# Kernel optimization log

Measured on AMD Instinct MI355X. Metric: run time of the kernel, lower is better.

The kernel has to match this reference:

```python
import jax, jax.numpy as jnp
import numpy as np
from functools import partial

DT = 1e-3
TAU_SYN_INV = 200.0  # norse default 1/5e-3
TAU_MEM_INV = 100.0  # norse default 1/1e-2

@partial(jax.custom_vjp, nondiff_argnums=(1,))
def superspike(x, alpha):
    return (x > 0).astype(x.dtype)

def _ss_fwd(x, alpha):
    return (x > 0).astype(x.dtype), x

def _ss_bwd(alpha, x, g):
    return (g / (alpha * jnp.abs(x) + 1.0) ** 2,)

superspike.defvjp(_ss_fwd, _ss_bwd)

def conv2d(x, w, b):
    y = jax.lax.conv_general_dilated(x, w, (1, 1), 'VALID',
                                     dimension_numbers=('NCHW', 'OIHW', 'NCHW'))
    return y + b[None, :, None, None]

def maxpool3(x):
    return jax.lax.reduce_window(x, -jnp.inf, jax.lax.max,
                                 (1, 1, 3, 3), (1, 1, 3, 3), 'VALID')

def lif_ff(inp, state, v_th, alpha):
    # norse feed-forward LIF: decay v and i, spike, reset, inject input current
    v, i = state
    v_dec = v + DT * TAU_MEM_INV * (-v + i)   # v_leak = 0
    i_dec = i - DT * TAU_SYN_INV * i
    z = superspike(v_dec - v_th, alpha)
    v_new = (1.0 - z) * v_dec                  # v_reset = 0
    return z, (v_new, i_dec + inp)

def lif_rec(inp, state, w_in, w_rec, v_th, alpha):
    # norse recurrent LIF: recurrent current uses PREVIOUS step's spikes
    z, v, i = state
    v_dec = v + DT * TAU_MEM_INV * (-v + i)
    i_dec = i - DT * TAU_SYN_INV * i
    z_new = superspike(v_dec - v_th, alpha)
    v_new = (1.0 - z_new) * v_dec
    i_new = i_dec + inp @ w_in.T + z @ w_rec.T
    return z_new, (z_new, v_new, i_new)

def li(inp, state):
    # leaky integrator readout (no spiking)
    v, i = state
    v_new = v + DT * TAU_MEM_INV * (-v + i)
    i_new = i - DT * TAU_SYN_INV * i + inp
    return v_new, (v_new, i_new)

def setup_inputs() -> dict:
    key = jax.random.key(0)
    ks = jax.random.split(key, 9)
    B, T, C, H, W = 32, 150, 2, 34, 34
    HID = 512
    x = jax.random.uniform(ks[0], (B, T, C, H, W), dtype=jnp.float32)
    def w(k, shape, fan_in):
        return jax.random.normal(k, shape, dtype=jnp.float32) / np.float32(np.sqrt(fan_in))
    return {
        'x': x,
        'conv1_w': w(ks[1], (30, 2, 7, 7), 2 * 49),
        'conv1_b': jnp.zeros((30,), jnp.float32),
        'conv2_w': w(ks[2], (70, 30, 5, 5), 30 * 25),
        'conv2_b': jnp.zeros((70,), jnp.float32),
        'l1_in_w': w(ks[3], (HID, 70), 70),
        'l1_rec_w': w(ks[4], (HID, HID), HID),
        'fc_out_w': w(ks[5], (4, HID), HID),
        'cl_in_w': w(ks[6], (2 * HID, 70), 70),
        'cl_rec_w': w(ks[7], (2 * HID, 2 * HID), 2 * HID),
        'cl_fc_w': w(ks[8], (10, 2 * HID), 2 * HID),
    }

def reference(x, conv1_w, conv1_b, conv2_w, conv2_b,
              l1_in_w, l1_rec_w, fc_out_w, cl_in_w, cl_rec_w, cl_fc_w):
    B = x.shape[0]
    HID = l1_in_w.shape[0]
    z0 = lambda *s: jnp.zeros(s, x.dtype)
    carry0 = (
        (z0(B, 30, 9, 9), z0(B, 30, 9, 9)),             # lif0 (v, i)
        (z0(B, 70, 1, 1), z0(B, 70, 1, 1)),             # lif1 (v, i)
        (z0(B, HID), z0(B, HID), z0(B, HID)),           # l1 (z, v, i)
        (z0(B, 4), z0(B, 4)),                            # out LI (v, i)
        (z0(B, 2 * HID), z0(B, 2 * HID), z0(B, 2 * HID)),# cl_l1 (z, v, i)
        (z0(B, 10), z0(B, 10)),                          # cl_out LI (v, i)
    )

    def step(carry, zt):
        s0, s2, s1, so, s1c, soc = carry
        z = maxpool3(conv2d(zt, conv1_w, conv1_b))       # (B,30,9,9)
        z, s0 = lif_ff(z, s0, 1.0, 100.0)
        z = maxpool3(conv2d(z, conv2_w, conv2_b))        # (B,70,1,1)
        z, s2 = lif_ff(z, s2, 1.0, 100.0)
        z = z.reshape(B, -1)                             # (B,70)
        z1, s1 = lif_rec(z, s1, l1_in_w, l1_rec_w, 0.4, 10.0)
        vo, so = li(z1 @ fc_out_w.T, so)
        z1c, s1c = lif_rec(z, s1c, cl_in_w, cl_rec_w, 0.4, 10.0)
        voc, soc = li(z1c @ cl_fc_w.T, soc)
        return (s0, s2, s1, so, s1c, soc), (vo, voc)

    _, (vos, vocs) = jax.lax.scan(step, carry0, jnp.swapaxes(x, 0, 1))
    y_hat = jnp.max(vos, axis=0)                         # (B,4)
    log_probs = jax.nn.log_softmax(jnp.max(vocs, axis=0), axis=1)  # (B,10)
    return y_hat, log_probs
```

## Files before the change

kernel.cpp:

```cpp
#include <hip/hip_runtime.h>
#include <math.h>


#define BATCH 32
#define TSTEPS 150
#define C1N 1470
#define ZSEQN 70
#define HID1 512
#define HID2 1024
#define K1CAT 582
#define K2CAT 1094

#define N_W1T  (K1CAT*HID1)
#define N_W2T  (K2CAT*HID2)

#define A1_U64  (BATCH*TSTEPS*32)
#define A0_U64  (BATCH*TSTEPS*16)
#define AC_U64  (BATCH*TSTEPS*8)
#define N_ARCH_U64 (A1_U64+A0_U64+AC_U64)

typedef unsigned long long u64;

__global__ void setup_misc(const float* __restrict__ l1_in_w,
                           const float* __restrict__ l1_rec_w,
                           const float* __restrict__ cl_in_w,
                           const float* __restrict__ cl_rec_w,
                           float* __restrict__ w1t,
                           float* __restrict__ w2t,
                           u64* __restrict__ arch) {
    int idx = blockIdx.x * blockDim.x + threadIdx.x;
    int stride = gridDim.x * blockDim.x;
    for (int e = idx; e < N_W1T; e += stride) {
        int j = e / HID1, o = e - j * HID1;
        w1t[e] = (j < HID1) ? l1_rec_w[o * HID1 + j] : l1_in_w[o * 70 + (j - HID1)];
    }
    for (int e = idx; e < N_W2T; e += stride) {
        int j = e / HID2, o = e - j * HID2;
        w2t[e] = (j < HID2) ? cl_rec_w[o * HID2 + j] : cl_in_w[o * 70 + (j - HID2)];
    }
    for (int e = idx; e < N_ARCH_U64; e += stride) arch[e] = 0ull;
}

__global__ __launch_bounds__(640) void conv1_pool(const float* __restrict__ x,
                                                  const float* __restrict__ w1,
                                                  const float* __restrict__ b1,
                                                  float* __restrict__ c1buf,
                                                  int b0) {
    __shared__ float img[2 * 34 * 34];
    __shared__ float w1s[30 * 2 * 49];
    __shared__ float crow[630 * 21];
    int tid = threadIdx.x;
    for (int e = tid; e < 2940; e += 640) w1s[e] = w1[e];
    #pragma unroll
    for (int k = 0; k < 2; ++k) {
        int f = blockIdx.x * 2 + k;
        int bl = f / TSTEPS, ts = f - bl * TSTEPS;
        const float* xin = x + ((size_t)(b0 + bl) * TSTEPS + ts) * 2312;
        __syncthreads();
        for (int e = tid; e < 2312; e += 640) img[e] = xin[e];
        __syncthreads();
        if (tid < 630) {
            int oc = tid / 21, cy = tid - oc * 21;
            float acc[21];
            #pragma unroll
            for (int j = 0; j < 21; ++j) acc[j] = 0.f;
            #pragma unroll
            for (int ic = 0; ic < 2; ++ic) {
                const float* irow0 = &img[ic * 1156];
                const float* wrow = &w1s[(oc * 2 + ic) * 49];
                #pragma unroll
                for (int ky = 0; ky < 7; ++ky) {
                    const float* ir = &irow0[(cy + ky) * 34];
                    float r[27];
                    #pragma unroll
                    for (int j = 0; j < 27; ++j) r[j] = ir[j];
                    #pragma unroll
                    for (int kx = 0; kx < 7; ++kx) {
                        float w = wrow[ky * 7 + kx];
                        #pragma unroll
                        for (int cx = 0; cx < 21; ++cx)
                            acc[cx] = fmaf(r[cx + kx], w, acc[cx]);
                    }
                }
            }
            #pragma unroll
            for (int cx = 0; cx < 21; ++cx) crow[tid * 21 + cx] = acc[cx];
        }
        __syncthreads();
        float* c1 = c1buf + (size_t)f * C1N;
        for (int p = tid; p < C1N; p += 640) {
            int oc = p / 49; int r = p - oc * 49; int py = r / 7, px = r - py * 7;
            float m = -1e30f;
            #pragma unroll
            for (int dy = 0; dy < 3; ++dy) {
                int rowid = oc * 21 + 3 * py + dy;
                #pragma unroll
                for (int dx = 0; dx < 3; ++dx)
                    m = fmaxf(m, crow[rowid * 21 + 3 * px + dx]);
            }
            c1[p] = m + b1[oc];
        }
    }
}

__device__ __forceinline__ float4 f4add(float4 a, const float4 b) {
    a.x += b.x; a.y += b.y; a.z += b.z; a.w += b.w; return a;
}
__device__ __forceinline__ void ast64(u64* p, u64 v) {
    __hip_atomic_store(p, v, __ATOMIC_RELAXED, __HIP_MEMORY_SCOPE_AGENT);
}
__device__ __forceinline__ u64 ald64(const u64* p) {
    return __hip_atomic_load((u64*)p, __ATOMIC_RELAXED, __HIP_MEMORY_SCOPE_AGENT);
}

__device__ __forceinline__ void conv_body(int w, int bl,
        const float* __restrict__ w2, const float* __restrict__ b2,
        const float* __restrict__ c1buf,
        u64* __restrict__ ac, float* smem) {
    const int ocStart2 = w * 9;
    const int nOc2 = (w == 7) ? 7 : 9;
    float* z0f  = smem;
    float* part = smem + 1472;
    float* red  = smem + 3904;

    const int t = threadIdx.x;
    float v0r[6], i0r[6], cf[6];
    #pragma unroll
    for (int k = 0; k < 6; ++k) { v0r[k] = 0.f; i0r[k] = 0.f; }
    float v2 = 0.f, i2 = 0.f;
    float bias2 = (t < nOc2) ? b2[ocStart2 + t] : 0.f;
    const float* c1 = c1buf + (size_t)bl * TSTEPS * C1N;
    #pragma unroll
    for (int k = 0; k < 6; ++k) {
        int e = t + k * 256;
        cf[k] = (e < C1N) ? c1[e] : 0.f;
    }
    if (t == 0) ast64(ac + w, ((u64)1 << 32));
    __syncthreads();

    for (int tt = 0; tt < TSTEPS; ++tt) {
        float nf[6];
        bool h = (tt + 1 < TSTEPS);
        if (h) {
            const float* c1n = c1 + (size_t)(tt + 1) * C1N;
            #pragma unroll
            for (int k = 0; k < 6; ++k) {
                int e = t + k * 256;
                nf[k] = (e < C1N) ? c1n[e] : 0.f;
            }
        }
        #pragma unroll
        for (int k = 0; k < 6; ++k) {
            int e = t + k * 256;
            if (e < C1N) {
                float vd = v0r[k] + 0.1f * (i0r[k] - v0r[k]);
                bool sp = (vd > 1.0f);
                v0r[k] = sp ? 0.f : vd;
                i0r[k] = i0r[k] - 0.2f * i0r[k] + cf[k];
                z0f[e] = sp ? 1.f : 0.f;
            }
        }
        __syncthreads();
        #pragma unroll
        for (int pass = 0; pass < 2; ++pass) {
            int u = t + pass * 256;
            if (u < nOc2 * 30) {
                int ol = u / 30, ic = u - ol * 30;
                float zw[49];
                #pragma unroll
                for (int j = 0; j < 49; ++j) zw[j] = z0f[ic * 49 + j];
                float a[9];
                #pragma unroll
                for (int p = 0; p < 9; ++p) a[p] = 0.f;
                const float* wb = w2 + (size_t)(ocStart2 + ol) * 750 + ic * 25;
                #pragma unroll
                for (int ky = 0; ky < 5; ++ky)
                    #pragma unroll
                    for (int kx = 0; kx < 5; ++kx) {
                        float wvv = wb[ky * 5 + kx];
                        #pragma unroll
                        for (int cy = 0; cy < 3; ++cy)
                            #pragma unroll
                            for (int cx = 0; cx < 3; ++cx)
                                a[cy * 3 + cx] = fmaf(zw[(cy + ky) * 7 + cx + kx], wvv, a[cy * 3 + cx]);
                    }
                #pragma unroll
                for (int p = 0; p < 9; ++p) part[u * 9 + p] = a[p];
            }
        }
        __syncthreads();
        if (t < nOc2 * 9) {
            int ol = t / 9, pos = t - ol * 9;
            float s2 = 0.f;
            for (int ic = 0; ic < 30; ++ic) s2 += part[(ol * 30 + ic) * 9 + pos];
            red[t] = s2;
        }
        __syncthreads();
        bool sp2 = false;
        if (t < nOc2) {
            float m = -1e30f;
            #pragma unroll
            for (int p = 0; p < 9; ++p) m = fmaxf(m, red[t * 9 + p]);
            float inp = m + bias2;
            float id2 = i2 - 0.2f * i2;
            i2 = id2 + inp;
            float vd2 = v2 + 0.1f * (i2 - v2);
            sp2 = (vd2 > 1.0f);
            v2 = sp2 ? 0.f : vd2;
        }
        if (tt + 1 < TSTEPS) {
            u64 mz2 = __ballot(sp2);
            if (t == 0)
                ast64(ac + (size_t)(tt + 1) * 8 + w,
                      (((u64)(tt + 2)) << 32) | (mz2 & 0x1ffull));
        }
        #pragma unroll
        for (int k = 0; k < 6; ++k) cf[k] = nf[k];
    }
}

template <int ROLE>
__device__ __forceinline__ void stripe_body(int b, int s,
        const float* __restrict__ catT,
        u64* __restrict__ arch,
        const u64* __restrict__ ac,
        float* smem) {
    constexpr int N    = ROLE ? HID2 : HID1;
    constexpr int K    = ROLE ? K2CAT : K1CAT;
    constexpr int SW   = N / 32;
    constexpr int NW   = N / 32;
    constexpr int NWT  = NW + 3;
    constexpr int N4   = N / 4;
    constexpr int COLS = ROLE ? 64 : 128;
    constexpr int QC   = COLS / 4;
    constexpr int S    = 256 / QC;
    constexpr int PSTR = COLS + 4;

    float* part = smem;
    unsigned short* list = (unsigned short*)(smem + 1088);
    unsigned int* maskw = (unsigned int*)(smem + 1088 + 547);
    unsigned int* wprefix = maskw + 40;

    const int t = threadIdx.x;
    const int lane = t & 63, wv = t >> 6;
    const int aid = t / QC, qid = t - (t / QC) * QC;
    const int q0 = s * QC;

    const float4* __restrict__ catT4 = (const float4*)catT;
    float v = 0.f, iacc = 0.f;

    if (wv == 0) {
        bool needc = (lane >= 40 && lane < 48);
        u64 cw = 0;
        for (;;) {
            if (needc) cw = ald64(ac + (lane - 40));
            bool ok = !needc || (unsigned)(cw >> 32) == 1u;
            if (__ballot(ok) == ~0ull) break;
            __builtin_amdgcn_s_sleep(1);
        }
        if (lane < NW) maskw[lane] = 0u;
        u64 lo = 0, hi = 0;
        #pragma unroll
        for (int w = 0; w < 8; ++w) {
            u64 p = (u64)(__shfl((unsigned)cw, 40 + w) & 0x1ffu);
            if (w < 7) lo |= p << (9 * w);
            else { lo |= (p & 1ull) << 63; hi = p >> 1; }
        }
        if (lane == 0) {
            maskw[NW] = (unsigned)lo; maskw[NW + 1] = (unsigned)(lo >> 32);
            maskw[NW + 2] = (unsigned)hi;
        }
        unsigned val = (lane < NWT) ? __popc(maskw[lane]) : 0u;
        #pragma unroll
        for (int d = 1; d < 64; d <<= 1) {
            unsigned u2 = __shfl_up(val, d);
            if (lane >= d) val += u2;
        }
        if (lane < NWT) wprefix[lane + 1] = val;
        if (lane == 0) wprefix[0] = 0u;
    }
    __syncthreads();
    int A = wprefix[NWT];
    for (int jj = t; jj < K; jj += 256) {
        unsigned m = maskw[jj >> 5];
        if ((m >> (jj & 31)) & 1u)
            list[wprefix[jj >> 5] + __popc(m & ((1u << (jj & 31)) - 1u))] = (unsigned short)jj;
    }
    __syncthreads();

    for (int tt = 0; tt < TSTEPS; ++tt) {
        float vd = v + 0.1f * (iacc - v);
        bool sp = (t < COLS) && (vd > 0.4f);
        float znew = sp ? 1.f : 0.f;
        if (t < COLS) v = sp ? 0.f : vd;
        u64 mz = __ballot(znew != 0.f);
        if (lane == 0 && wv < COLS / 64) {
            u64 tag = ((u64)(tt + 1)) << 32;
            u64* wslot = arch + (size_t)tt * SW + s * (COLS / 32) + wv * 2;
            ast64(wslot,     tag | (unsigned)(mz & 0xffffffffull));
            ast64(wslot + 1, tag | (unsigned)(mz >> 32));
        }
        float4 s0 = {0.f, 0.f, 0.f, 0.f}, s1 = s0, s2 = s0, s3 = s0;
        int idx = aid;
        for (; idx + 3 * S < A; idx += 4 * S) {
            s0 = f4add(s0, catT4[(size_t)list[idx]         * N4 + q0 + qid]);
            s1 = f4add(s1, catT4[(size_t)list[idx + S]     * N4 + q0 + qid]);
            s2 = f4add(s2, catT4[(size_t)list[idx + 2 * S] * N4 + q0 + qid]);
            s3 = f4add(s3, catT4[(size_t)list[idx + 3 * S] * N4 + q0 + qid]);
        }
        for (; idx < A; idx += S) s0 = f4add(s0, catT4[(size_t)list[idx] * N4 + q0 + qid]);
        s0 = f4add(f4add(s0, s1), f4add(s2, s3));
        *(float4*)(part + aid * PSTR + 4 * qid) = s0;
        __syncthreads();
        if (t < COLS) {
            float cur = 0.f;
            #pragma unroll
            for (int a = 0; a < S; ++a) cur += part[a * PSTR + t];
            iacc = iacc - 0.2f * iacc + cur;
        }
        if (tt + 1 >= TSTEPS) break;
        if (wv == 0) {
            bool needr = lane < SW;
            bool needc = (lane >= 40 && lane < 48);
            u64 wr = 0, wc = 0;
            for (;;) {
                if (needr) wr = ald64(arch + (size_t)tt * SW + lane);
                if (needc) wc = ald64(ac + (size_t)(tt + 1) * 8 + (lane - 40));
                bool ok = (!needr || (unsigned)(wr >> 32) == (unsigned)(tt + 1))
                       && (!needc || (unsigned)(wc >> 32) == (unsigned)(tt + 2));
                if (__ballot(ok) == ~0ull) break;
                __builtin_amdgcn_s_sleep(1);
            }
            if (needr) maskw[lane] = (unsigned)wr;
            u64 lo = 0, hi = 0;
            #pragma unroll
            for (int w = 0; w < 8; ++w) {
                u64 p = (u64)(__shfl((unsigned)wc, 40 + w) & 0x1ffu);
                if (w < 7) lo |= p << (9 * w);
                else { lo |= (p & 1ull) << 63; hi = p >> 1; }
            }
            if (lane == 0) {
                maskw[NW] = (unsigned)lo; maskw[NW + 1] = (unsigned)(lo >> 32);
                maskw[NW + 2] = (unsigned)hi;
            }
            unsigned val = (lane < NWT) ? __popc(maskw[lane]) : 0u;
            #pragma unroll
            for (int d = 1; d < 64; d <<= 1) {
                unsigned u2 = __shfl_up(val, d);
                if (lane >= d) val += u2;
            }
            if (lane < NWT) wprefix[lane + 1] = val;
            if (lane == 0) wprefix[0] = 0u;
        }
        __syncthreads();
        A = wprefix[NWT];
        for (int jj = t; jj < K; jj += 256) {
            unsigned m = maskw[jj >> 5];
            if ((m >> (jj & 31)) & 1u)
                list[wprefix[jj >> 5] + __popc(m & ((1u << (jj & 31)) - 1u))] = (unsigned short)jj;
        }
        __syncthreads();
    }
}

template <int ROLE>
__device__ __forceinline__ void readout_body(int b,
        const float* __restrict__ fcw,
        const u64* __restrict__ arch,
        float* __restrict__ out, float* smem) {
    constexpr int N  = ROLE ? HID2 : HID1;
    constexpr int SW = N / 32;
    constexpr int R  = ROLE ? 10 : 4;

    unsigned int* zw = (unsigned int*)smem;
    float* wpart = smem + 32;
    float* mvals = smem + 72;

    const int t = threadIdx.x;
    const int lane = t & 63, wv = t >> 6;
    float vli = 0.f, ili = 0.f, rmax = -1e30f;

    for (int tt = 0; tt < TSTEPS; ++tt) {
        if (wv == 0) {
            bool need = lane < SW;
            u64 w = 0;
            for (;;) {
                if (need) w = ald64(arch + (size_t)tt * SW + lane);
                bool ok = !need || (unsigned)(w >> 32) == (unsigned)(tt + 1);
                if (__ballot(ok) == ~0ull) break;
                __builtin_amdgcn_s_sleep(1);
            }
            if (need) zw[lane] = (unsigned)w;
        }
        __syncthreads();
        #pragma unroll
        for (int k = 0; k < R; ++k) {
            float p;
            if (ROLE) {
                unsigned bits = (zw[(t * 4) >> 5] >> ((t * 4) & 31)) & 0xFu;
                float4 w4 = ((const float4*)fcw)[k * (N / 4) + t];
                p = (bits & 1u ? w4.x : 0.f) + (bits & 2u ? w4.y : 0.f)
                  + (bits & 4u ? w4.z : 0.f) + (bits & 8u ? w4.w : 0.f);
            } else {
                unsigned bits = (zw[(t * 2) >> 5] >> ((t * 2) & 31)) & 0x3u;
                float2 w2 = ((const float2*)fcw)[k * (N / 2) + t];
                p = (bits & 1u ? w2.x : 0.f) + (bits & 2u ? w2.y : 0.f);
            }
            #pragma unroll
            for (int off = 32; off; off >>= 1) p += __shfl_xor(p, off);
            if (lane == 0) wpart[k * 4 + wv] = p;
        }
        __syncthreads();
        if (t < R) {
            float inp = wpart[t * 4] + wpart[t * 4 + 1] + wpart[t * 4 + 2] + wpart[t * 4 + 3];
            float vn = vli + 0.1f * (ili - vli);
            ili = ili - 0.2f * ili + inp;
            vli = vn;
            rmax = fmaxf(rmax, vn);
        }
    }
    if (ROLE) {
        if (t < 10) mvals[t] = rmax;
        __syncthreads();
        if (t < 10) {
            float M = -1e30f;
            #pragma unroll
            for (int k = 0; k < 10; ++k) M = fmaxf(M, mvals[k]);
            float ssum = 0.f;
            #pragma unroll
            for (int k = 0; k < 10; ++k) ssum += expf(mvals[k] - M);
            out[BATCH * 4 + b * 10 + t] = mvals[t] - M - logf(ssum);
        }
    } else if (t < 4) {
        out[b * 4 + t] = rmax;
    }
}

__global__ __launch_bounds__(256, 4) void snn_fused(
        const float* __restrict__ w2, const float* __restrict__ b2,
        const float* __restrict__ fc_out_w, const float* __restrict__ cl_fc_w,
        const float* __restrict__ w1t, const float* __restrict__ w2t,
        const float* __restrict__ c1buf,
        u64* __restrict__ arch1, u64* __restrict__ arch0,
        u64* __restrict__ archc,
        float* __restrict__ out, int b0, int BP) {
    __shared__ float smem[4096];
    int bid = blockIdx.x;
    if (bid < 8 * BP) {
        int w = bid / BP, bl = bid - w * BP;
        int b = b0 + bl;
        conv_body(w, bl, w2, b2, c1buf,
                  archc + (size_t)b * TSTEPS * 8, smem);
    } else if (bid < 24 * BP) {
        int idx = bid - 8 * BP;
        int s = idx / BP, bl = idx - s * BP;
        int b = b0 + bl;
        stripe_body<1>(b, s, w2t, arch1 + (size_t)b * TSTEPS * 32,
                       archc + (size_t)b * TSTEPS * 8, smem);
    } else if (bid < 28 * BP) {
        int idx = bid - 24 * BP;
        int s = idx / BP, bl = idx - s * BP;
        int b = b0 + bl;
        stripe_body<0>(b, s, w1t, arch0 + (size_t)b * TSTEPS * 16,
                       archc + (size_t)b * TSTEPS * 8, smem);
    } else if (bid < 29 * BP) {
        int b = b0 + (bid - 28 * BP);
        readout_body<1>(b, cl_fc_w, arch1 + (size_t)b * TSTEPS * 32, out, smem);
    } else {
        int b = b0 + (bid - 29 * BP);
        readout_body<0>(b, fc_out_w, arch0 + (size_t)b * TSTEPS * 16, out, smem);
    }
}

extern "C" void kernel_launch(void* const* d_in, const int* in_sizes, int n_in,
                              void* d_out, int out_size, void* d_ws, size_t ws_size,
                              hipStream_t stream) {
    const float* x        = (const float*)d_in[0];
    const float* w1       = (const float*)d_in[1];
    const float* b1       = (const float*)d_in[2];
    const float* w2       = (const float*)d_in[3];
    const float* b2       = (const float*)d_in[4];
    const float* l1_in_w  = (const float*)d_in[5];
    const float* l1_rec_w = (const float*)d_in[6];
    const float* fc_out_w = (const float*)d_in[7];
    const float* cl_in_w  = (const float*)d_in[8];
    const float* cl_rec_w = (const float*)d_in[9];
    const float* cl_fc_w  = (const float*)d_in[10];
    float* out = (float*)d_out;

    u64* arch1  = (u64*)d_ws;
    u64* arch0  = arch1 + A1_U64;
    u64* archc  = arch0 + A0_U64;
    float* w1t  = (float*)(archc + AC_U64);
    float* w2t  = w1t + N_W1T;
    float* c1buf = w2t + N_W2T;

    size_t head = 2 * (size_t)N_ARCH_U64 + N_W1T + N_W2T;
    size_t avail = ws_size / 4;
    int BP = 4;
    if (head + (size_t)32 * TSTEPS * C1N <= avail) BP = 32;
    else if (head + (size_t)16 * TSTEPS * C1N <= avail) BP = 16;
    else if (head + (size_t)8 * TSTEPS * C1N <= avail) BP = 8;

    setup_misc<<<dim3(256), dim3(256), 0, stream>>>(l1_in_w, l1_rec_w,
                                                    cl_in_w, cl_rec_w,
                                                    w1t, w2t, arch1);
    for (int b0 = 0; b0 < BATCH; b0 += BP) {
        conv1_pool<<<dim3(BP * TSTEPS / 2), dim3(640), 0, stream>>>(x, w1, b1, c1buf, b0);
        snn_fused<<<dim3(30 * BP), dim3(256), 0, stream>>>(w2, b2, fc_out_w, cl_fc_w,
                                                           w1t, w2t, c1buf,
                                                           arch1, arch0, archc,
                                                           out, b0, BP);
    }
}
```

Measured before the change: 719.8 us.

## Fuse conv1 front-end into persistent pipeline kernel with bit-packed spike flags

```diff
diff --git a/kernel.cpp b/kernel.cpp
--- a/kernel.cpp
+++ b/kernel.cpp
@@ -4,7 +4,6 @@
 
 #define BATCH 32
 #define TSTEPS 150
-#define C1N 1470
 #define ZSEQN 70
 #define HID1 512
 #define HID2 1024
@@ -17,7 +16,8 @@
 #define A1_U64  (BATCH*TSTEPS*32)
 #define A0_U64  (BATCH*TSTEPS*16)
 #define AC_U64  (BATCH*TSTEPS*8)
-#define N_ARCH_U64 (A1_U64+A0_U64+AC_U64)
+#define AZ_U64  (BATCH*TSTEPS*48)
+#define N_ARCH_U64 (A1_U64+A0_U64+AC_U64+AZ_U64)
 
 typedef unsigned long long u64;
 
@@ -41,36 +41,98 @@
     for (int e = idx; e < N_ARCH_U64; e += stride) arch[e] = 0ull;
 }
 
-__global__ __launch_bounds__(640) void conv1_pool(const float* __restrict__ x,
-                                                  const float* __restrict__ w1,
-                                                  const float* __restrict__ b1,
-                                                  float* __restrict__ c1buf,
-                                                  int b0) {
-    __shared__ float img[2 * 34 * 34];
-    __shared__ float w1s[30 * 2 * 49];
-    __shared__ float crow[630 * 21];
-    int tid = threadIdx.x;
-    for (int e = tid; e < 2940; e += 640) w1s[e] = w1[e];
+__device__ __forceinline__ float4 f4add(float4 a, const float4 b) {
+    a.x += b.x; a.y += b.y; a.z += b.z; a.w += b.w; return a;
+}
+__device__ __forceinline__ void ast64(u64* p, u64 v) {
+    __hip_atomic_store(p, v, __ATOMIC_RELAXED, __HIP_MEMORY_SCOPE_AGENT);
+}
+__device__ __forceinline__ u64 ald64(const u64* p) {
+    return __hip_atomic_load((u64*)p, __ATOMIC_RELAXED, __HIP_MEMORY_SCOPE_AGENT);
+}
+
+__device__ __forceinline__ void front_body(int h, int b,
+        const float* __restrict__ x, const float* __restrict__ w1,
+        const float* __restrict__ b1, u64* __restrict__ az, float* smem) {
+    float* img  = smem;
+    float* w1s  = smem + 2380;
+    float* part = smem + 3360;
+    unsigned int* zbu = (unsigned int*)(smem + 7770);
+
+    const int t = threadIdx.x;
+    const int lane = t & 63, wv = t >> 6;
+    const int oc0 = 10 * h;
+    const int ocl = t / 21, rem = t - ocl * 21;
+    const int cpy = rem / 3, cdy = rem - cpy * 3;
+    const int cy = 3 * cpy + cdy;
+    const float b1r = (t < 70) ? b1[oc0 + t / 7] : 0.f;
+
+    for (int e = t; e < 980; e += 256) w1s[e] = w1[oc0 * 98 + e];
+    float v0r[7], i0r[7];
     #pragma unroll
-    for (int k = 0; k < 2; ++k) {
-        int f = blockIdx.x * 2 + k;
-        int bl = f / TSTEPS, ts = f - bl * TSTEPS;
-        const float* xin = x + ((size_t)(b0 + bl) * TSTEPS + ts) * 2312;
-        __syncthreads();
-        for (int e = tid; e < 2312; e += 640) img[e] = xin[e];
-        __syncthreads();
-        if (tid < 630) {
-            int oc = tid / 21, cy = tid - oc * 21;
+    for (int k = 0; k < 7; ++k) { v0r[k] = 0.f; i0r[k] = 0.f; }
+
+    const float* xb = x + (size_t)b * TSTEPS * 2312;
+    float pf[10];
+    #pragma unroll
+    for (int k = 0; k < 10; ++k) {
+        int e = t + k * 256;
+        pf[k] = (e < 2312) ? xb[e] : 0.f;
+    }
+
+    for (int tt = 0; tt < TSTEPS; ++tt) {
+        if (t < 70) {
+            unsigned zbits = 0;
+            #pragma unroll
+            for (int px = 0; px < 7; ++px) {
+                float vd = v0r[px] + 0.1f * (i0r[px] - v0r[px]);
+                bool sp = (vd > 1.0f);
+                v0r[px] = sp ? 0.f : vd;
+                i0r[px] = i0r[px] - 0.2f * i0r[px];
+                zbits |= (sp ? 1u : 0u) << px;
+            }
+            zbu[t] = zbits;
+        }
+        __syncthreads();
+        if (wv == 0 && lane < 16) {
+            unsigned val = 0;
+            int tl0 = (32 * lane) / 7, tl1 = (32 * lane + 31) / 7;
+            for (int tl = tl0; tl <= tl1 && tl < 70; ++tl) {
+                int sh = 7 * tl - 32 * lane;
+                unsigned zb = zbu[tl] & 0x7Fu;
+                val |= (sh >= 0) ? (zb << sh) : (zb >> (-sh));
+            }
+            ast64(az + (size_t)tt * 48 + h * 16 + lane,
+                  (((u64)(tt + 1)) << 32) | val);
+        }
+        #pragma unroll
+        for (int k = 0; k < 10; ++k) {
+            int e = t + k * 256;
+            if (e < 2312) {
+                int ic = e / 1156, rr = e - ic * 1156;
+                img[ic * 1190 + (rr / 34) * 35 + (rr - 34 * (rr / 34))] = pf[k];
+            }
+        }
+        if (tt + 1 < TSTEPS) {
+            const float* xn = xb + (size_t)(tt + 1) * 2312;
+            #pragma unroll
+            for (int k = 0; k < 10; ++k) {
+                int e = t + k * 256;
+                pf[k] = (e < 2312) ? xn[e] : 0.f;
+            }
+        }
+        __syncthreads();
+        if (t < 210) {
             float acc[21];
             #pragma unroll
             for (int j = 0; j < 21; ++j) acc[j] = 0.f;
             #pragma unroll
             for (int ic = 0; ic < 2; ++ic) {
-                const float* irow0 = &img[ic * 1156];
-                const float* wrow = &w1s[(oc * 2 + ic) * 49];
+                const float* irow0 = &img[ic * 1190];
+                const float* wrow = &w1s[(ocl * 2 + ic) * 49];
                 #pragma unroll
                 for (int ky = 0; ky < 7; ++ky) {
-                    const float* ir = &irow0[(cy + ky) * 34];
+                    const float* ir = &irow0[(cy + ky) * 35];
                     float r[27];
                     #pragma unroll
                     for (int j = 0; j < 27; ++j) r[j] = ir[j];
@@ -84,81 +146,70 @@
                 }
             }
             #pragma unroll
-            for (int cx = 0; cx < 21; ++cx) crow[tid * 21 + cx] = acc[cx];
-        }
-        __syncthreads();
-        float* c1 = c1buf + (size_t)f * C1N;
-        for (int p = tid; p < C1N; p += 640) {
-            int oc = p / 49; int r = p - oc * 49; int py = r / 7, px = r - py * 7;
-            float m = -1e30f;
-            #pragma unroll
-            for (int dy = 0; dy < 3; ++dy) {
-                int rowid = oc * 21 + 3 * py + dy;
+            for (int cx = 0; cx < 21; ++cx) part[t * 21 + cx] = acc[cx];
+        }
+        __syncthreads();
+        if (t < 70) {
+            #pragma unroll
+            for (int px = 0; px < 7; ++px) {
+                float m = -1e30f;
                 #pragma unroll
-                for (int dx = 0; dx < 3; ++dx)
-                    m = fmaxf(m, crow[rowid * 21 + 3 * px + dx]);
-            }
-            c1[p] = m + b1[oc];
-        }
-    }
-}
-
-__device__ __forceinline__ float4 f4add(float4 a, const float4 b) {
-    a.x += b.x; a.y += b.y; a.z += b.z; a.w += b.w; return a;
-}
-__device__ __forceinline__ void ast64(u64* p, u64 v) {
-    __hip_atomic_store(p, v, __ATOMIC_RELAXED, __HIP_MEMORY_SCOPE_AGENT);
-}
-__device__ __forceinline__ u64 ald64(const u64* p) {
-    return __hip_atomic_load((u64*)p, __ATOMIC_RELAXED, __HIP_MEMORY_SCOPE_AGENT);
-}
-
-__device__ __forceinline__ void conv_body(int w, int bl,
+                for (int dy = 0; dy < 3; ++dy) {
+                    const float* row = &part[(t * 3 + dy) * 21];
+                    #pragma unroll
+                    for (int dx = 0; dx < 3; ++dx)
+                        m = fmaxf(m, row[3 * px + dx]);
+                }
+                i0r[px] = i0r[px] + (m + b1r);
+            }
+        }
+    }
+}
+
+__device__ __forceinline__ void conv_body(int w, int b,
         const float* __restrict__ w2, const float* __restrict__ b2,
-        const float* __restrict__ c1buf,
-        u64* __restrict__ ac, float* smem) {
+        const u64* __restrict__ az, u64* __restrict__ ac, float* smem) {
     const int ocStart2 = w * 9;
     const int nOc2 = (w == 7) ? 7 : 9;
     float* z0f  = smem;
     float* part = smem + 1472;
     float* red  = smem + 3904;
+    unsigned int* zwL = (unsigned int*)(smem + 3988);
 
     const int t = threadIdx.x;
-    float v0r[6], i0r[6], cf[6];
-    #pragma unroll
-    for (int k = 0; k < 6; ++k) { v0r[k] = 0.f; i0r[k] = 0.f; }
-    float v2 = 0.f, i2 = 0.f;
-    float bias2 = (t < nOc2) ? b2[ocStart2 + t] : 0.f;
-    const float* c1 = c1buf + (size_t)bl * TSTEPS * C1N;
+    const int lane = t & 63, wv = t >> 6;
+    int wI[6], bI[6];
     #pragma unroll
     for (int k = 0; k < 6; ++k) {
         int e = t + k * 256;
-        cf[k] = (e < C1N) ? c1[e] : 0.f;
-    }
+        if (e < 1470) {
+            int hh = e / 490, r = e - 490 * hh;
+            wI[k] = 16 * hh + (r >> 5);
+            bI[k] = r & 31;
+        } else { wI[k] = 0; bI[k] = 0; }
+    }
+    float v2 = 0.f, i2 = 0.f;
+    float bias2 = (t < nOc2) ? b2[ocStart2 + t] : 0.f;
     if (t == 0) ast64(ac + w, ((u64)1 << 32));
     __syncthreads();
 
     for (int tt = 0; tt < TSTEPS; ++tt) {
-        float nf[6];
-        bool h = (tt + 1 < TSTEPS);
-        if (h) {
-            const float* c1n = c1 + (size_t)(tt + 1) * C1N;
-            #pragma unroll
-            for (int k = 0; k < 6; ++k) {
-                int e = t + k * 256;
-                nf[k] = (e < C1N) ? c1n[e] : 0.f;
-            }
-        }
+        if (wv == 0) {
+            bool need = lane < 48;
+            u64 wd = 0;
+            for (;;) {
+                if (need) wd = ald64(az + (size_t)tt * 48 + lane);
+                bool ok = !need || (unsigned)(wd >> 32) == (unsigned)(tt + 1);
+                if (__ballot(ok) == ~0ull) break;
+                __builtin_amdgcn_s_sleep(1);
+            }
+            if (need) zwL[lane] = (unsigned)wd;
+        }
+        __syncthreads();
         #pragma unroll
         for (int k = 0; k < 6; ++k) {
             int e = t + k * 256;
-            if (e < C1N) {
-                float vd = v0r[k] + 0.1f * (i0r[k] - v0r[k]);
-                bool sp = (vd > 1.0f);
-                v0r[k] = sp ? 0.f : vd;
-                i0r[k] = i0r[k] - 0.2f * i0r[k] + cf[k];
-                z0f[e] = sp ? 1.f : 0.f;
-            }
+            if (e < 1470) z0f[e] = ((zwL[wI[k]] >> bI[k]) & 1u) ? 1.f : 0.f;
         }
         __syncthreads();
         #pragma unroll
@@ -214,8 +265,6 @@
                 ast64(ac + (size_t)(tt + 1) * 8 + w,
                       (((u64)(tt + 2)) << 32) | (mz2 & 0x1ffull));
         }
-        #pragma unroll
-        for (int k = 0; k < 6; ++k) cf[k] = nf[k];
     }
 }
 
@@ -363,112 +412,123 @@
     }
 }
 
-template <int ROLE>
-__device__ __forceinline__ void readout_body(int b,
-        const float* __restrict__ fcw,
-        const u64* __restrict__ arch,
+__device__ __forceinline__ void reader_body(int b,
+        const float* __restrict__ fc_out_w,
+        const float* __restrict__ cl_fc_w,
+        const u64* __restrict__ a1b, const u64* __restrict__ a0b,
         float* __restrict__ out, float* smem) {
-    constexpr int N  = ROLE ? HID2 : HID1;
-    constexpr int SW = N / 32;
-    constexpr int R  = ROLE ? 10 : 4;
-
-    unsigned int* zw = (unsigned int*)smem;
-    float* wpart = smem + 32;
-    float* mvals = smem + 72;
+    unsigned int* zw1 = (unsigned int*)smem;
+    unsigned int* zw0 = (unsigned int*)smem + 32;
+    float* wp1 = smem + 48;
+    float* wp0 = smem + 88;
+    float* mvals = smem + 104;
 
     const int t = threadIdx.x;
     const int lane = t & 63, wv = t >> 6;
-    float vli = 0.f, ili = 0.f, rmax = -1e30f;
+    const bool need1 = (wv == 0) && lane < 32;
+    const bool need0 = (wv == 0) && lane >= 32 && lane < 48;
+    float vli1 = 0.f, ili1 = 0.f, rmax1 = -1e30f;
+    float vli0 = 0.f, ili0 = 0.f, rmax0 = -1e30f;
 
     for (int tt = 0; tt < TSTEPS; ++tt) {
         if (wv == 0) {
-            bool need = lane < SW;
-            u64 w = 0;
+            u64 w1v = 0, w0v = 0;
             for (;;) {
-                if (need) w = ald64(arch + (size_t)tt * SW + lane);
-                bool ok = !need || (unsigned)(w >> 32) == (unsigned)(tt + 1);
+                if (need1) w1v = ald64(a1b + (size_t)tt * 32 + lane);
+                if (need0) w0v = ald64(a0b + (size_t)tt * 16 + (lane - 32));
+                bool ok = (!need1 || (unsigned)(w1v >> 32) == (unsigned)(tt + 1))
+                       && (!need0 || (unsigned)(w0v >> 32) == (unsigned)(tt + 1));
                 if (__ballot(ok) == ~0ull) break;
                 __builtin_amdgcn_s_sleep(1);
             }
-            if (need) zw[lane] = (unsigned)w;
-        }
-        __syncthreads();
-        #pragma unroll
-        for (int k = 0; k < R; ++k) {
-            float p;
-            if (ROLE) {
-                unsigned bits = (zw[(t * 4) >> 5] >> ((t * 4) & 31)) & 0xFu;
-                float4 w4 = ((const float4*)fcw)[k * (N / 4) + t];
-                p = (bits & 1u ? w4.x : 0.f) + (bits & 2u ? w4.y : 0.f)
-                  + (bits & 4u ? w4.z : 0.f) + (bits & 8u ? w4.w : 0.f);
-            } else {
-                unsigned bits = (zw[(t * 2) >> 5] >> ((t * 2) & 31)) & 0x3u;
-                float2 w2 = ((const float2*)fcw)[k * (N / 2) + t];
-                p = (bits & 1u ? w2.x : 0.f) + (bits & 2u ? w2.y : 0.f);
-            }
+            if (need1) zw1[lane] = (unsigned)w1v;
+            if (need0) zw0[lane - 32] = (unsigned)w0v;
+        }
+        __syncthreads();
+        #pragma unroll
+        for (int k = 0; k < 10; ++k) {
+            unsigned bits = (zw1[(t * 4) >> 5] >> ((t * 4) & 31)) & 0xFu;
+            float4 w4 = ((const float4*)cl_fc_w)[k * (HID2 / 4) + t];
+            float p = (bits & 1u ? w4.x : 0.f) + (bits & 2u ? w4.y : 0.f)
+                    + (bits & 4u ? w4.z : 0.f) + (bits & 8u ? w4.w : 0.f);
             #pragma unroll
             for (int off = 32; off; off >>= 1) p += __shfl_xor(p, off);
-            if (lane == 0) wpart[k * 4 + wv] = p;
-        }
-        __syncthreads();
-        if (t < R) {
-            float inp = wpart[t * 4] + wpart[t * 4 + 1] + wpart[t * 4 + 2] + wpart[t * 4 + 3];
-            float vn = vli + 0.1f * (ili - vli);
-            ili = ili - 0.2f * ili + inp;
-            vli = vn;
-            rmax = fmaxf(rmax, vn);
-        }
-    }
-    if (ROLE) {
-        if (t < 10) mvals[t] = rmax;
+            if (lane == 0) wp1[k * 4 + wv] = p;
+        }
+        #pragma unroll
+        for (int k = 0; k < 4; ++k) {
+            unsigned bits = (zw0[(t * 2) >> 5] >> ((t * 2) & 31)) & 0x3u;
+            float2 w2 = ((const float2*)fc_out_w)[k * (HID1 / 2) + t];
+            float p = (bits & 1u ? w2.x : 0.f) + (bits & 2u ? w2.y : 0.f);
+            #pragma unroll
+            for (int off = 32; off; off >>= 1) p += __shfl_xor(p, off);
+            if (lane == 0) wp0[k * 4 + wv] = p;
+        }
         __syncthreads();
         if (t < 10) {
-            float M = -1e30f;
-            #pragma unroll
-            for (int k = 0; k < 10; ++k) M = fmaxf(M, mvals[k]);
-            float ssum = 0.f;
-            #pragma unroll
-            for (int k = 0; k < 10; ++k) ssum += expf(mvals[k] - M);
-            out[BATCH * 4 + b * 10 + t] = mvals[t] - M - logf(ssum);
-        }
-    } else if (t < 4) {
-        out[b * 4 + t] = rmax;
-    }
+            float inp = wp1[t * 4] + wp1[t * 4 + 1] + wp1[t * 4 + 2] + wp1[t * 4 + 3];
+            float vn = vli1 + 0.1f * (ili1 - vli1);
+            ili1 = ili1 - 0.2f * ili1 + inp;
+            vli1 = vn;
+            rmax1 = fmaxf(rmax1, vn);
+        }
+        if (t >= 32 && t < 36) {
+            int r = t - 32;
+            float inp = wp0[r * 4] + wp0[r * 4 + 1] + wp0[r * 4 + 2] + wp0[r * 4 + 3];
+            float vn = vli0 + 0.1f * (ili0 - vli0);
+            ili0 = ili0 - 0.2f * ili0 + inp;
+            vli0 = vn;
+            rmax0 = fmaxf(rmax0, vn);
+        }
+    }
+    if (t < 10) mvals[t] = rmax1;
+    __syncthreads();
+    if (t < 10) {
+        float M = -1e30f;
+        #pragma unroll
+        for (int k = 0; k < 10; ++k) M = fmaxf(M, mvals[k]);
+        float ssum = 0.f;
+        #pragma unroll
+        for (int k = 0; k < 10; ++k) ssum += expf(mvals[k] - M);
+        out[BATCH * 4 + b * 10 + t] = mvals[t] - M - logf(ssum);
+    }
+    if (t >= 32 && t < 36) out[b * 4 + (t - 32)] = rmax0;
 }
 
 __global__ __launch_bounds__(256, 4) void snn_fused(
+        const float* __restrict__ x,
+        const float* __restrict__ w1, const float* __restrict__ b1,
         const float* __restrict__ w2, const float* __restrict__ b2,
         const float* __restrict__ fc_out_w, const float* __restrict__ cl_fc_w,
         const float* __restrict__ w1t, const float* __restrict__ w2t,
-        const float* __restrict__ c1buf,
         u64* __restrict__ arch1, u64* __restrict__ arch0,
-        u64* __restrict__ archc,
-        float* __restrict__ out, int b0, int BP) {
-    __shared__ float smem[4096];
+        u64* __restrict__ archc, u64* __restrict__ archz,
+        float* __restrict__ out) {
+    __shared__ float smem[7936];
     int bid = blockIdx.x;
-    if (bid < 8 * BP) {
-        int w = bid / BP, bl = bid - w * BP;
-        int b = b0 + bl;
-        conv_body(w, bl, w2, b2, c1buf,
+    if (bid < 96) {
+        int h = bid >> 5, b = bid & 31;
+        front_body(h, b, x, w1, b1, archz + (size_t)b * TSTEPS * 48, smem);
+    } else if (bid < 352) {
+        int idx = bid - 96;
+        int w = idx >> 5, b = idx & 31;
+        conv_body(w, b, w2, b2, archz + (size_t)b * TSTEPS * 48,
                   archc + (size_t)b * TSTEPS * 8, smem);
-    } else if (bid < 24 * BP) {
-        int idx = bid - 8 * BP;
-        int s = idx / BP, bl = idx - s * BP;
-        int b = b0 + bl;
+    } else if (bid < 864) {
+        int idx = bid - 352;
+        int s = idx & 15, b = idx >> 4;
         stripe_body<1>(b, s, w2t, arch1 + (size_t)b * TSTEPS * 32,
                        archc + (size_t)b * TSTEPS * 8, smem);
-    } else if (bid < 28 * BP) {
-        int idx = bid - 24 * BP;
-        int s = idx / BP, bl = idx - s * BP;
-        int b = b0 + bl;
+    } else if (bid < 992) {
+        int idx = bid - 864;
+        int s = idx & 3, b = idx >> 2;
         stripe_body<0>(b, s, w1t, arch0 + (size_t)b * TSTEPS * 16,
                        archc + (size_t)b * TSTEPS * 8, smem);
-    } else if (bid < 29 * BP) {
-        int b = b0 + (bid - 28 * BP);
-        readout_body<1>(b, cl_fc_w, arch1 + (size_t)b * TSTEPS * 32, out, smem);
     } else {
-        int b = b0 + (bid - 29 * BP);
-        readout_body<0>(b, fc_out_w, arch0 + (size_t)b * TSTEPS * 16, out, smem);
+        int b = bid - 992;
+        reader_body(b, fc_out_w, cl_fc_w,
+                    arch1 + (size_t)b * TSTEPS * 32,
+                    arch0 + (size_t)b * TSTEPS * 16, out, smem);
     }
 }
 
@@ -491,25 +551,14 @@
     u64* arch1  = (u64*)d_ws;
     u64* arch0  = arch1 + A1_U64;
     u64* archc  = arch0 + A0_U64;
-    float* w1t  = (float*)(archc + AC_U64);
+    u64* archz  = archc + AC_U64;
+    float* w1t  = (float*)(archz + AZ_U64);
     float* w2t  = w1t + N_W1T;
-    float* c1buf = w2t + N_W2T;
-
-    size_t head = 2 * (size_t)N_ARCH_U64 + N_W1T + N_W2T;
-    size_t avail = ws_size / 4;
-    int BP = 4;
-    if (head + (size_t)32 * TSTEPS * C1N <= avail) BP = 32;
-    else if (head + (size_t)16 * TSTEPS * C1N <= avail) BP = 16;
-    else if (head + (size_t)8 * TSTEPS * C1N <= avail) BP = 8;
 
     setup_misc<<<dim3(256), dim3(256), 0, stream>>>(l1_in_w, l1_rec_w,
                                                     cl_in_w, cl_rec_w,
                                                     w1t, w2t, arch1);
-    for (int b0 = 0; b0 < BATCH; b0 += BP) {
-        conv1_pool<<<dim3(BP * TSTEPS / 2), dim3(640), 0, stream>>>(x, w1, b1, c1buf, b0);
-        snn_fused<<<dim3(30 * BP), dim3(256), 0, stream>>>(w2, b2, fc_out_w, cl_fc_w,
-                                                           w1t, w2t, c1buf,
-                                                           arch1, arch0, archc,
-                                                           out, b0, BP);
-    }
-}
+    snn_fused<<<dim3(1024), dim3(256), 0, stream>>>(x, w1, b1, w2, b2,
+                                                    fc_out_w, cl_fc_w, w1t, w2t,
+                                                    arch1, arch0, archc, archz, out);
+}
```

Result: slower. 1.289 ms (+79.1%).
